# Kernel optimization log

Hardware: AMD Instinct MI355X
Metric: run time of the kernel (lower is better)

Reference implementation:

```python
import jax, jax.numpy as jnp
import numpy as np

EMBED = 256
HEADS = 8
SR = 2
RED = 2


def setup_inputs() -> dict:
    key = jax.random.key(0)
    ks = jax.random.split(key, 12)
    N, B, C = 1024, 64, EMBED
    inp = {
        "query": jax.random.normal(ks[0], (N, B, C), jnp.float32),
        "H": 32,
        "W": 32,
        "key": jax.random.normal(ks[1], (N, B, C), jnp.float32),
        "value": jax.random.normal(ks[2], (N, B, C), jnp.float32),
        # parameters
        "in_proj_weight": jax.random.normal(ks[3], (3 * C, C), jnp.float32) * (1.0 / np.sqrt(C)),
        "in_proj_bias": jnp.zeros((3 * C,), jnp.float32),
        "sr_w": jax.random.normal(ks[4], (C, C, SR, SR), jnp.float32) * np.sqrt(2.0 / (SR * SR * C)),
        "sr_b": jnp.zeros((C,), jnp.float32),
        "norm_g": jnp.ones((C,), jnp.float32),
        "norm_b": jnp.zeros((C,), jnp.float32),
        "out_w": jax.random.normal(ks[5], (C, C), jnp.float32) * (1.0 / np.sqrt(C)),
        "out_b": jnp.zeros((C,), jnp.float32),
        "se_w1": jax.random.normal(ks[6], (C // RED, C), jnp.float32) * 0.02,
        "se_w2": jax.random.normal(ks[7], (C, C // RED), jnp.float32) * 0.02,
    }
    return inp


def _angles(H, W):
    # get_index: a = (pi/2)*(i//W)/H, b = (pi/2)*(i%W)/W for flattened row-major index
    c = np.pi / 2
    idx = jnp.arange(H * W)
    a = c * (idx // W).astype(jnp.float32) / H
    b = c * (idx % W).astype(jnp.float32) / W
    return a, b


def _layernorm(x, g, b, eps=1e-5):
    mu = jnp.mean(x, -1, keepdims=True)
    var = jnp.mean(jnp.square(x - mu), -1, keepdims=True)
    return (x - mu) * jax.lax.rsqrt(var + eps) * g + b


def _abs_clamp(t, lo=1e-4, hi=1e4):
    return jnp.clip(jnp.abs(t), lo, hi) * jnp.sign(t)


def reference(query, H, W, key, value, in_proj_weight, in_proj_bias, sr_w, sr_b,
              norm_g, norm_b, out_w, out_b, se_w1, se_w2):
    N, B, C = query.shape
    h = HEADS
    hd = C // h
    scaling = hd ** (-0.5)

    x = jnp.transpose(query, (1, 0, 2))  # (B, N, C)

    # squeeze-excite gate from query: mean over tokens -> fc1 -> relu -> fc2 -> sigmoid
    se = jnp.mean(x, axis=1)                       # (B, C)
    se = jax.nn.sigmoid(jax.nn.relu(se @ se_w1.T) @ se_w2.T)  # (B, C)

    # spatial reduction conv (kernel=stride=sr_ratio) + layernorm for k/v source
    x_img = jnp.transpose(x, (0, 2, 1)).reshape(B, C, H, W)
    xr = jax.lax.conv_general_dilated(
        x_img, sr_w, window_strides=(SR, SR), padding="VALID",
        dimension_numbers=("NCHW", "OIHW", "NCHW"))
    xr = xr + sr_b[None, :, None, None]
    Hs, Ws = H // SR, W // SR
    Ns = Hs * Ws
    xr = jnp.transpose(xr.reshape(B, C, Ns), (0, 2, 1))  # (B, Ns, C)
    xr = _layernorm(xr, norm_g, norm_b)

    Wq, Wk, Wv = in_proj_weight[:C], in_proj_weight[C:2 * C], in_proj_weight[2 * C:]
    bq, bk, bv = in_proj_bias[:C], in_proj_bias[C:2 * C], in_proj_bias[2 * C:]

    def split_heads(t):  # (B, L, C) -> (B*h, L, hd)
        Bb, L, _ = t.shape
        return jnp.transpose(t.reshape(Bb, L, h, hd), (0, 2, 1, 3)).reshape(Bb * h, L, hd)

    q = split_heads((x @ Wq.T + bq) * scaling)
    k = split_heads(xr @ Wk.T + bk)
    v = split_heads(xr @ Wv.T + bv)

    q = jax.nn.relu(q)
    k = jax.nn.relu(k)

    # cosFormer-2d "sum" reweighting: cos(a_i - a_j) + cos(b_i - b_j)
    a, b = _angles(H, W)       # (N,)
    a2, b2 = _angles(Hs, Ws)   # (Ns,)

    def reweight(t, aa, bb):  # (BH, L, hd), angles (L,) -> (BH, L, 4*hd)
        aa = aa[None, :, None]
        bb = bb[None, :, None]
        return jnp.concatenate(
            [t * jnp.cos(aa), t * jnp.sin(aa), t * jnp.cos(bb), t * jnp.sin(bb)], axis=-1)

    q_ = reweight(q, a, b)     # (BH, N, 4hd)
    k_ = reweight(k, a2, b2)   # (BH, Ns, 4hd)

    # linear attention: never materialize the NxNs matrix
    kv = jnp.einsum("bnd,bnm->bdm", k_, v)             # (BH, 4hd, hd)
    denom = jnp.einsum("bnd,bd->bn", q_, k_.sum(1))    # (BH, N)
    denom = _abs_clamp(denom)
    attn = jnp.einsum("bnd,bdm->bnm", q_, kv) / denom[..., None]  # (BH, N, hd)

    attn = jnp.transpose(attn.reshape(B, h, N, hd), (0, 2, 1, 3)).reshape(B, N, C)
    out = attn @ out_w.T + out_b            # (B, N, C)
    out = out * se[:, None, :]              # SE channel gating
    return jnp.transpose(out, (1, 0, 2))    # (N, B, C)
```

## Files before the change

kernel.cpp:

```cpp
#include <hip/hip_runtime.h>

#define NTOK 1024
#define NB   64
#define CD   256
#define NHEAD 8
#define HDIM 32
#define NS 256
#define NBC 16384

typedef __attribute__((ext_vector_type(8))) short short8v;
typedef __attribute__((ext_vector_type(4))) short short4v;
typedef __attribute__((ext_vector_type(4))) float f32x4;

__device__ __forceinline__ unsigned bfr(float x){
  unsigned u = __float_as_uint(x);
  return (u + 0x7fffu + ((u>>16)&1u)) >> 16;
}
__device__ __forceinline__ void split2(float x, short &h, short &l){
  unsigned hu = bfr(x);
  float hf = __uint_as_float(hu << 16);
  unsigned lu = bfr(x - hf);
  h = (short)hu; l = (short)lu;
}

__global__ __launch_bounds__(256) void k_pre(const float* __restrict__ ipw, const float* __restrict__ ow,
                                             const float* __restrict__ srw,
                                             short* __restrict__ Wih, short* __restrict__ Wil,
                                             short* __restrict__ Woh, short* __restrict__ Wol,
                                             short* __restrict__ Wsh, short* __restrict__ Wsl,
                                             float* __restrict__ t1, float* __restrict__ t2,
                                             const float* __restrict__ query, float* __restrict__ part){
  int bid = blockIdx.x, t = threadIdx.x;
  if (bid < 256){
    int u = bid*256 + t;
    float xs[8];
    short* dh; short* dl; int dof;
    if (u < 24576){
      int n = u >> 5, off = (u & 31)*8;
      const float* s = ipw + n*CD + off;
      #pragma unroll
      for (int i=0;i<8;++i) xs[i] = s[i];
      dh = Wih; dl = Wil; dof = n*CD + off;
    } else if (u < 32768){
      int v = u - 24576;
      int n = v >> 5, off = (v & 31)*8;
      const float* s = ow + n*CD + off;
      #pragma unroll
      for (int i=0;i<8;++i) xs[i] = s[i];
      dh = Woh; dl = Wol; dof = n*CD + off;
    } else {
      int v = u - 32768;
      int n = v >> 7, koff = (v & 127)*8;
      int g = koff >> 8, cin0 = koff & 255;
      #pragma unroll
      for (int i=0;i<8;++i) xs[i] = srw[n*1024 + (cin0+i)*4 + g];
      dh = Wsh; dl = Wsl; dof = n*1024 + koff;
    }
    short8v h, l;
    #pragma unroll
    for (int i=0;i<8;++i){ short a,b; split2(xs[i],a,b); h[i]=a; l[i]=b; }
    *(short8v*)(dh + dof) = h;
    *(short8v*)(dl + dof) = l;
  } else if (bid < 260){
    int n = (bid-256)*256 + t;
    const float c = 1.57079632679489662f;
    float aa = c * (float)(n >> 5) / 32.0f;
    float bb = c * (float)(n & 31) / 32.0f;
    t1[n*4+0]=cosf(aa); t1[n*4+1]=sinf(aa); t1[n*4+2]=cosf(bb); t1[n*4+3]=sinf(bb);
    if (n < 256){
      float a2 = c * (float)(n >> 4) / 16.0f;
      float b2 = c * (float)(n & 15) / 16.0f;
      t2[n*4+0]=cosf(a2); t2[n*4+1]=sinf(a2); t2[n*4+2]=cosf(b2); t2[n*4+3]=sinf(b2);
    }
  } else {
    int vb_ = bid - 260;
    int b = vb_ >> 2, qr = vb_ & 3;
    const float* qp = query + (qr*256)*NBC + b*CD + t;
    float s0=0.f,s1=0.f,s2=0.f,s3=0.f;
    for (int n=0;n<256;n+=4){
      s0 += qp[(n  )*NBC];
      s1 += qp[(n+1)*NBC];
      s2 += qp[(n+2)*NBC];
      s3 += qp[(n+3)*NBC];
    }
    part[vb_*256 + t] = (s0+s1)+(s2+s3);
  }
}

__global__ __launch_bounds__(256) void k_mid(const float* __restrict__ qf,
                                             const short* __restrict__ Wsh, const short* __restrict__ Wsl,
                                             const float* __restrict__ srb, float* __restrict__ xr,
                                             const short* __restrict__ Wih, const short* __restrict__ Wil,
                                             const float* __restrict__ ipb,
                                             short* __restrict__ Qbh, short* __restrict__ Qbl,
                                             const float* __restrict__ part, const float* __restrict__ w1,
                                             const float* __restrict__ w2, float* __restrict__ se){
  __shared__ __align__(16) short smem[16384];
  int bid = blockIdx.x, t = threadIdx.x;
  if (bid < 512){
    short* Ah = smem;
    short* Al = smem + 2048;
    short* Bh = smem + 4096;
    short* Bl = smem + 8192;
    int mblk = bid >> 1, nblk = bid & 1;
    int m0 = mblk*64, n0 = nblk*128;
    int b = mblk >> 2;
    int pos0 = m0 & 255;
    int wave = t>>6, lane = t&63;
    int wm = wave>>1, wn = wave&1;
    int q = lane>>4, r = lane&15;
    int ra = t>>2, pa = (t&3)*8;
    int posA = pos0 + ra, hs = posA>>4, ws2 = posA&15;
    const f32x4 fz = {0.f,0.f,0.f,0.f};
    f32x4 acc[2][4];
    #pragma unroll
    for (int s=0;s<2;++s)
      #pragma unroll
      for (int tt=0;tt<4;++tt) acc[s][tt] = fz;
    for (int kc=0; kc<32; ++kc){
      int g = kc>>3, cin0 = (kc&7)*32;
      int gh = g>>1, gw = g&1;
      int tok = (2*hs+gh)*32 + 2*ws2 + gw;
      const float* src = qf + (size_t)tok*NBC + b*CD + cin0 + pa;
      float4 fa = *(const float4*)src;
      float4 fb = *(const float4*)(src+4);
      float xs[8] = {fa.x,fa.y,fa.z,fa.w,fb.x,fb.y,fb.z,fb.w};
      short8v hh, ll;
      #pragma unroll
      for (int i=0;i<8;++i){ short a0,b0; split2(xs[i],a0,b0); hh[i]=a0; ll[i]=b0; }
      *(short8v*)(Ah + ra*32 + pa) = hh;
      *(short8v*)(Al + ra*32 + pa) = ll;
      int ko = kc*32;
      #pragma unroll
      for (int rep=0; rep<2; ++rep){
        int rr = ra + rep*64;
        int gb = (n0 + rr)*1024 + ko + pa;
        *(short8v*)(Bh + rr*32 + pa) = *(const short8v*)(Wsh + gb);
        *(short8v*)(Bl + rr*32 + pa) = *(const short8v*)(Wsl + gb);
      }
      __syncthreads();
      short8v ah[2], al[2];
      #pragma unroll
      for (int s=0;s<2;++s){
        int row = wm*32 + s*16 + r;
        ah[s] = *(const short8v*)(Ah + row*32 + q*8);
        al[s] = *(const short8v*)(Al + row*32 + q*8);
      }
      #pragma unroll
      for (int tt=0;tt<4;++tt){
        int brow = wn*64 + tt*16 + r;
        short8v bh = *(const short8v*)(Bh + brow*32 + q*8);
        short8v bl = *(const short8v*)(Bl + brow*32 + q*8);
        #pragma unroll
        for (int s=0;s<2;++s){
          acc[s][tt] = __builtin_amdgcn_mfma_f32_16x16x32_bf16(ah[s], bh, acc[s][tt], 0,0,0);
          acc[s][tt] = __builtin_amdgcn_mfma_f32_16x16x32_bf16(ah[s], bl, acc[s][tt], 0,0,0);
          acc[s][tt] = __builtin_amdgcn_mfma_f32_16x16x32_bf16(al[s], bh, acc[s][tt], 0,0,0);
        }
      }
      __syncthreads();
    }
    #pragma unroll
    for (int s=0;s<2;++s){
      #pragma unroll
      for (int tt=0;tt<4;++tt){
        int c = n0 + wn*64 + tt*16 + r;
        float bias = srb[c];
        #pragma unroll
        for (int i=0;i<4;++i){
          int m = m0 + wm*32 + s*16 + q*4 + i;
          xr[m*CD + c] = acc[s][tt][i] + bias;
        }
      }
    }
  } else if (bid < 1536){
    short* Ah = smem;
    short* Al = smem + 4096;
    short* Bh = smem + 8192;
    short* Bl = smem + 12288;
    int qb_ = bid - 512;
    int mblk = qb_ >> 1, nblk = qb_ & 1;
    int m0 = mblk*128, n0 = nblk*128;
    int wave = t>>6, lane = t&63;
    int wm = wave>>1, wn = wave&1;
    int q = lane>>4, r = lane&15;
    int cr = t>>2, cp = (t&3)*8;
    int cpS = (((t&3) ^ ((cr>>1)&3)))*8;
    int sw8 = ((r>>1)&3)*8;
    const f32x4 fz = {0.f,0.f,0.f,0.f};
    f32x4 acc[4][4];
    #pragma unroll
    for (int s=0;s<4;++s)
      #pragma unroll
      for (int tt=0;tt<4;++tt) acc[s][tt] = fz;
    for (int kc=0; kc<8; ++kc){
      int ko = kc*32;
      #pragma unroll
      for (int rep=0; rep<2; ++rep){
        int rr = cr + rep*64;
        int m = m0 + rr;
        const float* src = qf + (size_t)(m & 1023)*NBC + (m >> 10)*CD + ko + cp;
        float4 fa = *(const float4*)src;
        float4 fb = *(const float4*)(src+4);
        float xs[8] = {fa.x,fa.y,fa.z,fa.w,fb.x,fb.y,fb.z,fb.w};
        short8v hh, ll;
        #pragma unroll
        for (int i=0;i<8;++i){ short a0,b0; split2(xs[i],a0,b0); hh[i]=a0; ll[i]=b0; }
        *(short8v*)(Ah + rr*32 + cpS) = hh;
        *(short8v*)(Al + rr*32 + cpS) = ll;
        int gb = (n0 + rr)*CD + ko + cp;
        *(short8v*)(Bh + rr*32 + cpS) = *(const short8v*)(Wih + gb);
        *(short8v*)(Bl + rr*32 + cpS) = *(const short8v*)(Wil + gb);
      }
      __syncthreads();
      short8v ah[4], al[4];
      #pragma unroll
      for (int s=0;s<4;++s){
        int row = wm*64 + s*16 + r;
        ah[s] = *(const short8v*)(Ah + row*32 + ((q*8)^sw8));
        al[s] = *(const short8v*)(Al + row*32 + ((q*8)^sw8));
      }
      #pragma unroll
      for (int tt=0;tt<4;++tt){
        int brow = wn*64 + tt*16 + r;
        short8v bh = *(const short8v*)(Bh + brow*32 + ((q*8)^sw8));
        short8v bl = *(const short8v*)(Bl + brow*32 + ((q*8)^sw8));
        #pragma unroll
        for (int s=0;s<4;++s){
          acc[s][tt] = __builtin_amdgcn_mfma_f32_16x16x32_bf16(ah[s], bh, acc[s][tt], 0,0,0);
          acc[s][tt] = __builtin_amdgcn_mfma_f32_16x16x32_bf16(ah[s], bl, acc[s][tt], 0,0,0);
          acc[s][tt] = __builtin_amdgcn_mfma_f32_16x16x32_bf16(al[s], bh, acc[s][tt], 0,0,0);
        }
      }
      __syncthreads();
    }
    const float sc = 0.17677669529663687f;
    short* T = smem;
    #pragma unroll
    for (int s=0;s<4;++s){
      #pragma unroll
      for (int tt=0;tt<4;++tt){
        int c_loc = wn*64 + tt*16 + r;
        int chunk = c_loc >> 3, cb = c_loc & 7;
        float bias = ipb[n0 + c_loc];
        #pragma unroll
        for (int i=0;i<4;++i){
          int m_loc = wm*64 + s*16 + q*4 + i;
          float val = fmaxf(acc[s][tt][i] + bias, 0.f)*sc;
          unsigned hu = bfr(val);
          T[m_loc*128 + ((chunk ^ (m_loc&7))<<3) + cb] = (short)hu;
          acc[s][tt][i] = val - __uint_as_float(hu<<16);
        }
      }
    }
    __syncthreads();
    {
      int mrl = (lane>>2);
      int ccl = lane&3;
      #pragma unroll
      for (int e=0;e<8;++e){
        int hl = e&3, mg = e>>2;
        int m_loc = wave*32 + mg*16 + mrl;
        int cc16 = hl*4 + ccl;
        short8v v = *(const short8v*)(T + m_loc*128 + ((cc16 ^ (m_loc&7))<<3));
        *(short8v*)(Qbh + ((size_t)((n0>>5)+hl))*2097152 + (size_t)(m0+m_loc)*32 + ccl*8) = v;
      }
    }
    __syncthreads();
    #pragma unroll
    for (int s=0;s<4;++s){
      #pragma unroll
      for (int tt=0;tt<4;++tt){
        int c_loc = wn*64 + tt*16 + r;
        int chunk = c_loc >> 3, cb = c_loc & 7;
        #pragma unroll
        for (int i=0;i<4;++i){
          int m_loc = wm*64 + s*16 + q*4 + i;
          T[m_loc*128 + ((chunk ^ (m_loc&7))<<3) + cb] = (short)bfr(acc[s][tt][i]);
        }
      }
    }
    __syncthreads();
    {
      int mrl = (lane>>2);
      int ccl = lane&3;
      #pragma unroll
      for (int e=0;e<8;++e){
        int hl = e&3, mg = e>>2;
        int m_loc = wave*32 + mg*16 + mrl;
        int cc16 = hl*4 + ccl;
        short8v v = *(const short8v*)(T + m_loc*128 + ((cc16 ^ (m_loc&7))<<3));
        *(short8v*)(Qbl + ((size_t)((n0>>5)+hl))*2097152 + (size_t)(m0+m_loc)*32 + ccl*8) = v;
      }
    }
  } else {
    float* sm = (float*)smem;
    float* s1s = sm + 256;
    int b = bid - 1536;
    float s = (part[(b*4+0)*256+t]+part[(b*4+1)*256+t])+(part[(b*4+2)*256+t]+part[(b*4+3)*256+t]);
    sm[t] = s*(1.0f/1024.0f);
    __syncthreads();
    if (t < 128){
      float a = 0.f;
      const float* wr = w1 + t*256;
      for (int c=0;c<256;c+=4){
        float4 wf = *(const float4*)(wr+c);
        a += sm[c]*wf.x + sm[c+1]*wf.y + sm[c+2]*wf.z + sm[c+3]*wf.w;
      }
      s1s[t] = fmaxf(a, 0.f);
    }
    __syncthreads();
    float a = 0.f;
    const float* wr2 = w2 + t*128;
    for (int c=0;c<128;c+=4){
      float4 wf = *(const float4*)(wr2+c);
      a += s1s[c]*wf.x + s1s[c+1]*wf.y + s1s[c+2]*wf.z + s1s[c+3]*wf.w;
    }
    se[b*256+t] = 1.0f/(1.0f+expf(-a));
  }
}

__global__ __launch_bounds__(256) void k_ln(const float* __restrict__ xr, const float* __restrict__ g,
                                            const float* __restrict__ bta, short* __restrict__ Xh,
                                            short* __restrict__ Xl){
  int wv = threadIdx.x >> 6, lane = threadIdx.x & 63;
  int row = blockIdx.x*4 + wv;
  float4 v = ((const float4*)(xr + row*CD))[lane];
  float s = (v.x+v.y)+(v.z+v.w);
  #pragma unroll
  for (int off=1; off<64; off<<=1) s += __shfl_xor(s, off, 64);
  float mu = s * (1.0f/256.0f);
  float dx=v.x-mu, dy=v.y-mu, dz=v.z-mu, dw=v.w-mu;
  float s2 = (dx*dx+dy*dy)+(dz*dz+dw*dw);
  #pragma unroll
  for (int off=1; off<64; off<<=1) s2 += __shfl_xor(s2, off, 64);
  float inv = 1.0f / sqrtf(s2*(1.0f/256.0f) + 1e-5f);
  float4 gr = ((const float4*)g)[lane];
  float4 br = ((const float4*)bta)[lane];
  float o0 = dx*inv*gr.x + br.x;
  float o1 = dy*inv*gr.y + br.y;
  float o2 = dz*inv*gr.z + br.z;
  float o3 = dw*inv*gr.w + br.w;
  short4v h, l; short a0,b0;
  split2(o0,a0,b0); h[0]=a0; l[0]=b0;
  split2(o1,a0,b0); h[1]=a0; l[1]=b0;
  split2(o2,a0,b0); h[2]=a0; l[2]=b0;
  split2(o3,a0,b0); h[3]=a0; l[3]=b0;
  *(short4v*)(Xh + row*CD + lane*4) = h;
  *(short4v*)(Xl + row*CD + lane*4) = l;
}

__global__ __launch_bounds__(256) void k_kvproj(const short* __restrict__ Xh, const short* __restrict__ Xl,
                                                const short* __restrict__ Wkh, const short* __restrict__ Wkl,
                                                const float* __restrict__ ipb, float* __restrict__ kb,
                                                float* __restrict__ vb){
  __shared__ __align__(16) short Ah[128*32];
  __shared__ __align__(16) short Al[128*32];
  __shared__ __align__(16) short Bh[128*32];
  __shared__ __align__(16) short Bl[128*32];
  int mblk = blockIdx.x >> 2, nblk = blockIdx.x & 3;
  int m0 = mblk*128, n0 = nblk*128;
  int t = threadIdx.x, wave = t>>6, lane = t&63;
  int wm = wave>>1, wn = wave&1;
  int q = lane>>4, r = lane&15;
  int cr = t>>2, cp = (t&3)*8;
  const f32x4 fz = {0.f,0.f,0.f,0.f};
  f32x4 acc[4][4];
  #pragma unroll
  for (int s=0;s<4;++s)
    #pragma unroll
    for (int tt=0;tt<4;++tt) acc[s][tt] = fz;
  for (int kc=0; kc<8; ++kc){
    int ko = kc*32;
    #pragma unroll
    for (int rep=0; rep<2; ++rep){
      int rr = cr + rep*64;
      int ga = (m0 + rr)*CD + ko + cp;
      *(short8v*)(Ah + rr*32 + cp) = *(const short8v*)(Xh + ga);
      *(short8v*)(Al + rr*32 + cp) = *(const short8v*)(Xl + ga);
      int gb = (n0 + rr)*CD + ko + cp;
      *(short8v*)(Bh + rr*32 + cp) = *(const short8v*)(Wkh + gb);
      *(short8v*)(Bl + rr*32 + cp) = *(const short8v*)(Wkl + gb);
    }
    __syncthreads();
    short8v ah[4], al[4];
    #pragma unroll
    for (int s=0;s<4;++s){
      int row = wm*64 + s*16 + r;
      ah[s] = *(const short8v*)(Ah + row*32 + q*8);
      al[s] = *(const short8v*)(Al + row*32 + q*8);
    }
    #pragma unroll
    for (int tt=0;tt<4;++tt){
      int brow = wn*64 + tt*16 + r;
      short8v bh = *(const short8v*)(Bh + brow*32 + q*8);
      short8v bl = *(const short8v*)(Bl + brow*32 + q*8);
      #pragma unroll
      for (int s=0;s<4;++s){
        acc[s][tt] = __builtin_amdgcn_mfma_f32_16x16x32_bf16(ah[s], bh, acc[s][tt], 0,0,0);
        acc[s][tt] = __builtin_amdgcn_mfma_f32_16x16x32_bf16(ah[s], bl, acc[s][tt], 0,0,0);
        acc[s][tt] = __builtin_amdgcn_mfma_f32_16x16x32_bf16(al[s], bh, acc[s][tt], 0,0,0);
      }
    }
    __syncthreads();
  }
  #pragma unroll
  for (int s=0;s<4;++s){
    #pragma unroll
    for (int tt=0;tt<4;++tt){
      int c = n0 + wn*64 + tt*16 + r;
      float bias = ipb[256 + c];
      #pragma unroll
      for (int i=0;i<4;++i){
        int m = m0 + wm*64 + s*16 + q*4 + i;
        float v = acc[s][tt][i] + bias;
        if (c < 256) kb[m*CD + c] = fmaxf(v, 0.f);
        else         vb[m*CD + (c-256)] = v;
      }
    }
  }
}

__global__ __launch_bounds__(256) void k_kvattn(const float* __restrict__ kb, const float* __restrict__ vbuf,
                                                const float* __restrict__ t2,
                                                const short* __restrict__ Qbh, const short* __restrict__ Qbl,
                                                const float* __restrict__ t1,
                                                short* __restrict__ Ath, short* __restrict__ Atl){
  __shared__ __align__(16) short Bh[144*32];
  __shared__ __align__(16) short Bl[144*32];
  __shared__ __align__(16) short Ah[256*32];
  __shared__ __align__(16) short Al[256*32];
  int bh = blockIdx.x, b = bh>>3, h = bh&7;
  int t = threadIdx.x, lane = t&63, wave = t>>6;
  int q = lane>>4, r = lane&15;
  {
    int jq = t >> 5, m = t & 31;
    float acc[4][4];
    #pragma unroll
    for (int p=0;p<4;++p){ acc[p][0]=0.f; acc[p][1]=0.f; acc[p][2]=0.f; acc[p][3]=0.f; }
    const float* kbase = kb + h*HDIM + jq*4;
    const float* vbase = vbuf + h*HDIM + m;
    for (int n=0;n<256;++n){
      int ro = (b*NS + n)*CD;
      float4 k4 = *(const float4*)(kbase + ro);
      float vv = vbase[ro];
      float4 tt = *(const float4*)(t2 + n*4);
      float tv[4] = {tt.x, tt.y, tt.z, tt.w};
      float kk[4] = {k4.x, k4.y, k4.z, k4.w};
      #pragma unroll
      for (int p=0;p<4;++p){
        float tp = tv[p]*vv;
        #pragma unroll
        for (int jj=0;jj<4;++jj) acc[p][jj] += tp*kk[jj];
      }
    }
    #pragma unroll
    for (int p=0;p<4;++p){
      short4v h4, l4;
      #pragma unroll
      for (int jj=0;jj<4;++jj){ short a,bq; split2(acc[p][jj],a,bq); h4[jj]=a; l4[jj]=bq; }
      *(short4v*)(Bh + (p*32+m)*32 + jq*4) = h4;
      *(short4v*)(Bl + (p*32+m)*32 + jq*4) = l4;
    }
    if (t < 128){
      int p = t >> 5, j = t & 31;
      float s=0.f;
      const float* kp = kb + h*HDIM + j;
      for (int n=0;n<256;++n) s += t2[n*4+p]*kp[(b*NS+n)*CD];
      short a,bq; split2(s,a,bq);
      Bh[(128+p)*32 + j] = a;
      Bl[(128+p)*32 + j] = bq;
    } else {
      int idx = t - 128;
      #pragma unroll
      for (int ii=0;ii<3;++ii){
        Bh[4224 + idx*3 + ii] = 0;
        Bl[4224 + idx*3 + ii] = 0;
      }
    }
  }
  __syncthreads();
  short8v bf_h[9], bf_l[9];
  #pragma unroll
  for (int nt=0; nt<9; ++nt){
    int row = nt*16 + r;
    bf_h[nt] = *(const short8v*)(Bh + row*32 + q*8);
    bf_l[nt] = *(const short8v*)(Bl + row*32 + q*8);
  }
  const short* qh_base = Qbh + ((size_t)h*65536 + (size_t)b*1024)*32;
  const short* ql_base = Qbl + ((size_t)h*65536 + (size_t)b*1024)*32;
  const f32x4 fz = {0.f,0.f,0.f,0.f};
  for (int u=0; u<4; ++u){
    __syncthreads();
    {
      const short8v* sh = (const short8v*)(qh_base + (u*256 + t)*32);
      const short8v* sl = (const short8v*)(ql_base + (u*256 + t)*32);
      short8v* dh = (short8v*)(Ah + t*32);
      short8v* dl = (short8v*)(Al + t*32);
      #pragma unroll
      for (int i=0;i<4;++i){ dh[i]=sh[i]; dl[i]=sl[i]; }
    }
    __syncthreads();
    #pragma unroll
    for (int mi=0; mi<4; ++mi){
      int mt = wave*4 + mi;
      short8v ah = *(const short8v*)(Ah + (mt*16 + r)*32 + q*8);
      short8v al = *(const short8v*)(Al + (mt*16 + r)*32 + q*8);
      f32x4 acc[9];
      #pragma unroll
      for (int nt=0;nt<9;++nt) acc[nt]=fz;
      #pragma unroll
      for (int nt=0;nt<9;++nt){
        acc[nt] = __builtin_amdgcn_mfma_f32_16x16x32_bf16(ah, bf_h[nt], acc[nt],0,0,0);
        acc[nt] = __builtin_amdgcn_mfma_f32_16x16x32_bf16(ah, bf_l[nt], acc[nt],0,0,0);
        acc[nt] = __builtin_amdgcn_mfma_f32_16x16x32_bf16(al, bf_h[nt], acc[nt],0,0,0);
      }
      int nbase = u*256 + mt*16 + q*4;
      int src = lane & 48;
      #pragma unroll
      for (int i=0;i<4;++i){
        int n = nbase + i;
        float4 tv = *(const float4*)(t1 + n*4);
        float dp0 = __shfl(acc[8][i], src+0, 64);
        float dp1 = __shfl(acc[8][i], src+1, 64);
        float dp2 = __shfl(acc[8][i], src+2, 64);
        float dp3 = __shfl(acc[8][i], src+3, 64);
        float den = tv.x*dp0 + tv.y*dp1 + tv.z*dp2 + tv.w*dp3;
        float a0 = tv.x*acc[0][i] + tv.y*acc[2][i] + tv.z*acc[4][i] + tv.w*acc[6][i];
        float a1 = tv.x*acc[1][i] + tv.y*acc[3][i] + tv.z*acc[5][i] + tv.w*acc[7][i];
        float sgn = (den>0.f) ? 1.f : ((den<0.f)? -1.f : 0.f);
        float ad = fminf(fmaxf(fabsf(den), 1e-4f), 1e4f);
        float inv = (den != 0.f) ? 1.0f/(ad*sgn) : 0.f;
        float o0 = a0*inv, o1 = a1*inv;
        int mrow = b*NTOK + n;
        short h0,l0,h1,l1;
        split2(o0,h0,l0); split2(o1,h1,l1);
        Ath[mrow*CD + h*HDIM + r]      = h0;
        Atl[mrow*CD + h*HDIM + r]      = l0;
        Ath[mrow*CD + h*HDIM + 16 + r] = h1;
        Atl[mrow*CD + h*HDIM + 16 + r] = l1;
      }
    }
  }
}

__global__ __launch_bounds__(256) void k_outproj(const short* __restrict__ Ath, const short* __restrict__ Atl,
                                                 const short* __restrict__ Woh, const short* __restrict__ Wol,
                                                 const float* __restrict__ obv, const float* __restrict__ se,
                                                 float* __restrict__ dout){
  __shared__ __align__(16) short Ah[128*32];
  __shared__ __align__(16) short Al[128*32];
  __shared__ __align__(16) short Bh[128*32];
  __shared__ __align__(16) short Bl[128*32];
  int mblk = blockIdx.x >> 1, nblk = blockIdx.x & 1;
  int m0 = mblk*128, n0 = nblk*128;
  int t = threadIdx.x, wave = t>>6, lane = t&63;
  int wm = wave>>1, wn = wave&1;
  int q = lane>>4, r = lane&15;
  int cr = t>>2, cp = (t&3)*8;
  const f32x4 fz = {0.f,0.f,0.f,0.f};
  f32x4 acc[4][4];
  #pragma unroll
  for (int s=0;s<4;++s)
    #pragma unroll
    for (int tt=0;tt<4;++tt) acc[s][tt] = fz;
  for (int kc=0; kc<8; ++kc){
    int ko = kc*32;
    #pragma unroll
    for (int rep=0; rep<2; ++rep){
      int rr = cr + rep*64;
      int ga = (m0 + rr)*CD + ko + cp;
      *(short8v*)(Ah + rr*32 + cp) = *(const short8v*)(Ath + ga);
      *(short8v*)(Al + rr*32 + cp) = *(const short8v*)(Atl + ga);
      int gb = (n0 + rr)*CD + ko + cp;
      *(short8v*)(Bh + rr*32 + cp) = *(const short8v*)(Woh + gb);
      *(short8v*)(Bl + rr*32 + cp) = *(const short8v*)(Wol + gb);
    }
    __syncthreads();
    short8v ah[4], al[4];
    #pragma unroll
    for (int s=0;s<4;++s){
      int row = wm*64 + s*16 + r;
      ah[s] = *(const short8v*)(Ah + row*32 + q*8);
      al[s] = *(const short8v*)(Al + row*32 + q*8);
    }
    #pragma unroll
    for (int tt=0;tt<4;++tt){
      int brow = wn*64 + tt*16 + r;
      short8v bh = *(const short8v*)(Bh + brow*32 + q*8);
      short8v bl = *(const short8v*)(Bl + brow*32 + q*8);
      #pragma unroll
      for (int s=0;s<4;++s){
        acc[s][tt] = __builtin_amdgcn_mfma_f32_16x16x32_bf16(ah[s], bh, acc[s][tt], 0,0,0);
        acc[s][tt] = __builtin_amdgcn_mfma_f32_16x16x32_bf16(ah[s], bl, acc[s][tt], 0,0,0);
        acc[s][tt] = __builtin_amdgcn_mfma_f32_16x16x32_bf16(al[s], bh, acc[s][tt], 0,0,0);
      }
    }
    __syncthreads();
  }
  #pragma unroll
  for (int s=0;s<4;++s){
    #pragma unroll
    for (int tt=0;tt<4;++tt){
      int c = n0 + wn*64 + tt*16 + r;
      float bias = obv[c];
      #pragma unroll
      for (int i=0;i<4;++i){
        int m = m0 + wm*64 + s*16 + q*4 + i;
        int bb = m >> 10, ntok = m & 1023;
        float sev = se[bb*CD + c];
        dout[(ntok*NB + bb)*CD + c] = (acc[s][tt][i] + bias)*sev;
      }
    }
  }
}

extern "C" void kernel_launch(void* const* d_in, const int* in_sizes, int n_in,
                              void* d_out, int out_size, void* d_ws, size_t ws_size,
                              hipStream_t stream) {
  const float* query = (const float*)d_in[0];
  const float* ipw = (const float*)d_in[5];
  const float* ipb = (const float*)d_in[6];
  const float* srw = (const float*)d_in[7];
  const float* srb = (const float*)d_in[8];
  const float* ng  = (const float*)d_in[9];
  const float* nbb = (const float*)d_in[10];
  const float* ow  = (const float*)d_in[11];
  const float* obv = (const float*)d_in[12];
  const float* sw1 = (const float*)d_in[13];
  const float* sw2 = (const float*)d_in[14];
  float* dout = (float*)d_out;
  float* ws = (float*)d_ws;

  short* Qbh  = (short*)ws;
  short* Qbl  = (short*)(ws + 8388608);
  float* R1   = ws + 16777216;
  float* kb   = R1;
  float* vb   = R1 + 4194304;
  short* Ath  = (short*)(R1 + 8388608);
  short* Atl  = (short*)(ws + 33554432);
  float* xr   = ws + 33554432;
  short* Xh   = (short*)(ws + 37748736);
  short* Xl   = (short*)(ws + 39845888);
  float* part = ws + 44302336;
  float* se   = ws + 44367872;
  float* t1   = ws + 44384256;
  float* t2   = ws + 44388352;
  short* Wih  = (short*)(ws + 44389376);
  short* Wil  = (short*)(ws + 44487680);
  short* Woh  = (short*)(ws + 44585984);
  short* Wol  = (short*)(ws + 44618752);
  short* Wsh  = (short*)(ws + 44651520);
  short* Wsl  = (short*)(ws + 44782592);

  k_pre   <<<516,  256,0,stream>>>(ipw, ow, srw, Wih, Wil, Woh, Wol, Wsh, Wsl, t1, t2, query, part);
  k_mid   <<<1600, 256,0,stream>>>(query, Wsh, Wsl, srb, xr, Wih, Wil, ipb, Qbh, Qbl, part, sw1, sw2, se);
  k_ln    <<<4096, 256,0,stream>>>(xr, ng, nbb, Xh, Xl);
  k_kvproj<<<512,  256,0,stream>>>(Xh, Xl, Wih + 256*CD, Wil + 256*CD, ipb, kb, vb);
  k_kvattn<<<512,  256,0,stream>>>(kb, vb, t2, Qbh, Qbl, t1, Ath, Atl);
  k_outproj<<<1024,256,0,stream>>>(Ath, Atl, Woh, Wol, obv, se, dout);
}
```

Baseline: 430.0 us.

## Fuse weight prep, layernorm, and SE into neighboring kernels to cut launches

Removes the separate weight-conversion prologue by having the SR-conv and Q-projection GEMMs split fp32 weights on the fly, and moves the remaining K/V/out weight conversion, angle tables and query partial sums into extra blocks of k_mid. LayerNorm is folded into k_kvproj, which computes per-row statistics and normalizes while staging A tiles, so the Xh/Xl intermediate is gone. The SE MLP moves into extra blocks of k_kvattn. This cuts the launch count from six to four and drops intermediate traffic, at the cost of redundant weight splitting per tile and strided srw loads.

```diff
diff --git a/kernel.cpp b/kernel.cpp
--- a/kernel.cpp
+++ b/kernel.cpp
@@ -23,78 +23,16 @@
   h = (short)hu; l = (short)lu;
 }
 
-__global__ __launch_bounds__(256) void k_pre(const float* __restrict__ ipw, const float* __restrict__ ow,
+__global__ __launch_bounds__(256) void k_mid(const float* __restrict__ qf,
                                              const float* __restrict__ srw,
+                                             const float* __restrict__ srb, float* __restrict__ xr,
+                                             const float* __restrict__ ipw, const float* __restrict__ ipb,
+                                             short* __restrict__ Qbh, short* __restrict__ Qbl,
+                                             const float* __restrict__ ow,
                                              short* __restrict__ Wih, short* __restrict__ Wil,
                                              short* __restrict__ Woh, short* __restrict__ Wol,
-                                             short* __restrict__ Wsh, short* __restrict__ Wsl,
                                              float* __restrict__ t1, float* __restrict__ t2,
-                                             const float* __restrict__ query, float* __restrict__ part){
-  int bid = blockIdx.x, t = threadIdx.x;
-  if (bid < 256){
-    int u = bid*256 + t;
-    float xs[8];
-    short* dh; short* dl; int dof;
-    if (u < 24576){
-      int n = u >> 5, off = (u & 31)*8;
-      const float* s = ipw + n*CD + off;
-      #pragma unroll
-      for (int i=0;i<8;++i) xs[i] = s[i];
-      dh = Wih; dl = Wil; dof = n*CD + off;
-    } else if (u < 32768){
-      int v = u - 24576;
-      int n = v >> 5, off = (v & 31)*8;
-      const float* s = ow + n*CD + off;
-      #pragma unroll
-      for (int i=0;i<8;++i) xs[i] = s[i];
-      dh = Woh; dl = Wol; dof = n*CD + off;
-    } else {
-      int v = u - 32768;
-      int n = v >> 7, koff = (v & 127)*8;
-      int g = koff >> 8, cin0 = koff & 255;
-      #pragma unroll
-      for (int i=0;i<8;++i) xs[i] = srw[n*1024 + (cin0+i)*4 + g];
-      dh = Wsh; dl = Wsl; dof = n*1024 + koff;
-    }
-    short8v h, l;
-    #pragma unroll
-    for (int i=0;i<8;++i){ short a,b; split2(xs[i],a,b); h[i]=a; l[i]=b; }
-    *(short8v*)(dh + dof) = h;
-    *(short8v*)(dl + dof) = l;
-  } else if (bid < 260){
-    int n = (bid-256)*256 + t;
-    const float c = 1.57079632679489662f;
-    float aa = c * (float)(n >> 5) / 32.0f;
-    float bb = c * (float)(n & 31) / 32.0f;
-    t1[n*4+0]=cosf(aa); t1[n*4+1]=sinf(aa); t1[n*4+2]=cosf(bb); t1[n*4+3]=sinf(bb);
-    if (n < 256){
-      float a2 = c * (float)(n >> 4) / 16.0f;
-      float b2 = c * (float)(n & 15) / 16.0f;
-      t2[n*4+0]=cosf(a2); t2[n*4+1]=sinf(a2); t2[n*4+2]=cosf(b2); t2[n*4+3]=sinf(b2);
-    }
-  } else {
-    int vb_ = bid - 260;
-    int b = vb_ >> 2, qr = vb_ & 3;
-    const float* qp = query + (qr*256)*NBC + b*CD + t;
-    float s0=0.f,s1=0.f,s2=0.f,s3=0.f;
-    for (int n=0;n<256;n+=4){
-      s0 += qp[(n  )*NBC];
-      s1 += qp[(n+1)*NBC];
-      s2 += qp[(n+2)*NBC];
-      s3 += qp[(n+3)*NBC];
-    }
-    part[vb_*256 + t] = (s0+s1)+(s2+s3);
-  }
-}
-
-__global__ __launch_bounds__(256) void k_mid(const float* __restrict__ qf,
-                                             const short* __restrict__ Wsh, const short* __restrict__ Wsl,
-                                             const float* __restrict__ srb, float* __restrict__ xr,
-                                             const short* __restrict__ Wih, const short* __restrict__ Wil,
-                                             const float* __restrict__ ipb,
-                                             short* __restrict__ Qbh, short* __restrict__ Qbl,
-                                             const float* __restrict__ part, const float* __restrict__ w1,
-                                             const float* __restrict__ w2, float* __restrict__ se){
+                                             float* __restrict__ part){
   __shared__ __align__(16) short smem[16384];
   int bid = blockIdx.x, t = threadIdx.x;
   if (bid < 512){
@@ -130,13 +68,15 @@
       for (int i=0;i<8;++i){ short a0,b0; split2(xs[i],a0,b0); hh[i]=a0; ll[i]=b0; }
       *(short8v*)(Ah + ra*32 + pa) = hh;
       *(short8v*)(Al + ra*32 + pa) = ll;
-      int ko = kc*32;
       #pragma unroll
       for (int rep=0; rep<2; ++rep){
         int rr = ra + rep*64;
-        int gb = (n0 + rr)*1024 + ko + pa;
-        *(short8v*)(Bh + rr*32 + pa) = *(const short8v*)(Wsh + gb);
-        *(short8v*)(Bl + rr*32 + pa) = *(const short8v*)(Wsl + gb);
+        const float* wsrc = srw + (size_t)(n0+rr)*1024 + (size_t)(cin0+pa)*4 + g;
+        short8v wh8, wl8;
+        #pragma unroll
+        for (int i=0;i<8;++i){ short a0,b0; split2(wsrc[i*4],a0,b0); wh8[i]=a0; wl8[i]=b0; }
+        *(short8v*)(Bh + rr*32 + pa) = wh8;
+        *(short8v*)(Bl + rr*32 + pa) = wl8;
       }
       __syncthreads();
       short8v ah[2], al[2];
@@ -208,9 +148,15 @@
         for (int i=0;i<8;++i){ short a0,b0; split2(xs[i],a0,b0); hh[i]=a0; ll[i]=b0; }
         *(short8v*)(Ah + rr*32 + cpS) = hh;
         *(short8v*)(Al + rr*32 + cpS) = ll;
-        int gb = (n0 + rr)*CD + ko + cp;
-        *(short8v*)(Bh + rr*32 + cpS) = *(const short8v*)(Wih + gb);
-        *(short8v*)(Bl + rr*32 + cpS) = *(const short8v*)(Wil + gb);
+        const float* wsrc = ipw + (size_t)(n0+rr)*CD + ko + cp;
+        float4 wa = *(const float4*)wsrc;
+        float4 wb = *(const float4*)(wsrc+4);
+        float wsv[8] = {wa.x,wa.y,wa.z,wa.w,wb.x,wb.y,wb.z,wb.w};
+        short8v wh8, wl8;
+        #pragma unroll
+        for (int i=0;i<8;++i){ short a0,b0; split2(wsv[i],a0,b0); wh8[i]=a0; wl8[i]=b0; }
+        *(short8v*)(Bh + rr*32 + cpS) = wh8;
+        *(short8v*)(Bl + rr*32 + cpS) = wl8;
       }
       __syncthreads();
       short8v ah[4], al[4];
@@ -293,64 +239,52 @@
         *(short8v*)(Qbl + ((size_t)((n0>>5)+hl))*2097152 + (size_t)(m0+m_loc)*32 + ccl*8) = v;
       }
     }
+  } else if (bid < 1632){
+    int u = (bid-1536)*256 + t;
+    const float* s; short* dh; short* dl; int dof;
+    if (u < 16384){
+      int n = 256 + (u >> 5), off = (u & 31)*8;
+      s = ipw + n*CD + off;
+      dh = Wih; dl = Wil; dof = n*CD + off;
+    } else {
+      int v = u - 16384;
+      int n = v >> 5, off = (v & 31)*8;
+      s = ow + n*CD + off;
+      dh = Woh; dl = Wol; dof = n*CD + off;
+    }
+    short8v h, l;
+    #pragma unroll
+    for (int i=0;i<8;++i){ short a,b; split2(s[i],a,b); h[i]=a; l[i]=b; }
+    *(short8v*)(dh + dof) = h;
+    *(short8v*)(dl + dof) = l;
+  } else if (bid < 1636){
+    int n = (bid-1632)*256 + t;
+    const float c = 1.57079632679489662f;
+    float aa = c * (float)(n >> 5) / 32.0f;
+    float bb = c * (float)(n & 31) / 32.0f;
+    t1[n*4+0]=cosf(aa); t1[n*4+1]=sinf(aa); t1[n*4+2]=cosf(bb); t1[n*4+3]=sinf(bb);
+    if (n < 256){
+      float a2 = c * (float)(n >> 4) / 16.0f;
+      float b2 = c * (float)(n & 15) / 16.0f;
+      t2[n*4+0]=cosf(a2); t2[n*4+1]=sinf(a2); t2[n*4+2]=cosf(b2); t2[n*4+3]=sinf(b2);
+    }
   } else {
-    float* sm = (float*)smem;
-    float* s1s = sm + 256;
-    int b = bid - 1536;
-    float s = (part[(b*4+0)*256+t]+part[(b*4+1)*256+t])+(part[(b*4+2)*256+t]+part[(b*4+3)*256+t]);
-    sm[t] = s*(1.0f/1024.0f);
-    __syncthreads();
-    if (t < 128){
-      float a = 0.f;
-      const float* wr = w1 + t*256;
-      for (int c=0;c<256;c+=4){
-        float4 wf = *(const float4*)(wr+c);
-        a += sm[c]*wf.x + sm[c+1]*wf.y + sm[c+2]*wf.z + sm[c+3]*wf.w;
-      }
-      s1s[t] = fmaxf(a, 0.f);
-    }
-    __syncthreads();
-    float a = 0.f;
-    const float* wr2 = w2 + t*128;
-    for (int c=0;c<128;c+=4){
-      float4 wf = *(const float4*)(wr2+c);
-      a += s1s[c]*wf.x + s1s[c+1]*wf.y + s1s[c+2]*wf.z + s1s[c+3]*wf.w;
-    }
-    se[b*256+t] = 1.0f/(1.0f+expf(-a));
+    int vb_ = bid - 1636;
+    int b = vb_ >> 2, qr = vb_ & 3;
+    const float* qp = qf + (qr*256)*NBC + b*CD + t;
+    float s0=0.f,s1=0.f,s2=0.f,s3=0.f;
+    for (int n=0;n<256;n+=4){
+      s0 += qp[(n  )*NBC];
+      s1 += qp[(n+1)*NBC];
+      s2 += qp[(n+2)*NBC];
+      s3 += qp[(n+3)*NBC];
+    }
+    part[vb_*256 + t] = (s0+s1)+(s2+s3);
   }
 }
 
-__global__ __launch_bounds__(256) void k_ln(const float* __restrict__ xr, const float* __restrict__ g,
-                                            const float* __restrict__ bta, short* __restrict__ Xh,
-                                            short* __restrict__ Xl){
-  int wv = threadIdx.x >> 6, lane = threadIdx.x & 63;
-  int row = blockIdx.x*4 + wv;
-  float4 v = ((const float4*)(xr + row*CD))[lane];
-  float s = (v.x+v.y)+(v.z+v.w);
-  #pragma unroll
-  for (int off=1; off<64; off<<=1) s += __shfl_xor(s, off, 64);
-  float mu = s * (1.0f/256.0f);
-  float dx=v.x-mu, dy=v.y-mu, dz=v.z-mu, dw=v.w-mu;
-  float s2 = (dx*dx+dy*dy)+(dz*dz+dw*dw);
-  #pragma unroll
-  for (int off=1; off<64; off<<=1) s2 += __shfl_xor(s2, off, 64);
-  float inv = 1.0f / sqrtf(s2*(1.0f/256.0f) + 1e-5f);
-  float4 gr = ((const float4*)g)[lane];
-  float4 br = ((const float4*)bta)[lane];
-  float o0 = dx*inv*gr.x + br.x;
-  float o1 = dy*inv*gr.y + br.y;
-  float o2 = dz*inv*gr.z + br.z;
-  float o3 = dw*inv*gr.w + br.w;
-  short4v h, l; short a0,b0;
-  split2(o0,a0,b0); h[0]=a0; l[0]=b0;
-  split2(o1,a0,b0); h[1]=a0; l[1]=b0;
-  split2(o2,a0,b0); h[2]=a0; l[2]=b0;
-  split2(o3,a0,b0); h[3]=a0; l[3]=b0;
-  *(short4v*)(Xh + row*CD + lane*4) = h;
-  *(short4v*)(Xl + row*CD + lane*4) = l;
-}
-
-__global__ __launch_bounds__(256) void k_kvproj(const short* __restrict__ Xh, const short* __restrict__ Xl,
+__global__ __launch_bounds__(256) void k_kvproj(const float* __restrict__ xr, const float* __restrict__ lng,
+                                                const float* __restrict__ lnb,
                                                 const short* __restrict__ Wkh, const short* __restrict__ Wkl,
                                                 const float* __restrict__ ipb, float* __restrict__ kb,
                                                 float* __restrict__ vb){
@@ -358,12 +292,29 @@
   __shared__ __align__(16) short Al[128*32];
   __shared__ __align__(16) short Bh[128*32];
   __shared__ __align__(16) short Bl[128*32];
+  __shared__ float mu_s[128];
+  __shared__ float inv_s[128];
   int mblk = blockIdx.x >> 2, nblk = blockIdx.x & 3;
   int m0 = mblk*128, n0 = nblk*128;
   int t = threadIdx.x, wave = t>>6, lane = t&63;
   int wm = wave>>1, wn = wave&1;
   int q = lane>>4, r = lane&15;
   int cr = t>>2, cp = (t&3)*8;
+  for (int rr8=0; rr8<32; ++rr8){
+    int rr = rr8*4 + wave;
+    float4 v = ((const float4*)(xr + (size_t)(m0+rr)*CD))[lane];
+    float s = (v.x+v.y)+(v.z+v.w);
+    #pragma unroll
+    for (int off=1; off<64; off<<=1) s += __shfl_xor(s, off, 64);
+    float mu = s * (1.0f/256.0f);
+    float dx=v.x-mu, dy=v.y-mu, dz=v.z-mu, dw=v.w-mu;
+    float s2 = (dx*dx+dy*dy)+(dz*dz+dw*dw);
+    #pragma unroll
+    for (int off=1; off<64; off<<=1) s2 += __shfl_xor(s2, off, 64);
+    float inv = 1.0f / sqrtf(s2*(1.0f/256.0f) + 1e-5f);
+    if (lane==0){ mu_s[rr]=mu; inv_s[rr]=inv; }
+  }
+  __syncthreads();
   const f32x4 fz = {0.f,0.f,0.f,0.f};
   f32x4 acc[4][4];
   #pragma unroll
@@ -375,9 +326,25 @@
     #pragma unroll
     for (int rep=0; rep<2; ++rep){
       int rr = cr + rep*64;
-      int ga = (m0 + rr)*CD + ko + cp;
-      *(short8v*)(Ah + rr*32 + cp) = *(const short8v*)(Xh + ga);
-      *(short8v*)(Al + rr*32 + cp) = *(const short8v*)(Xl + ga);
+      const float* src = xr + (size_t)(m0+rr)*CD + ko + cp;
+      float4 fa = *(const float4*)src;
+      float4 fb = *(const float4*)(src+4);
+      float xs[8] = {fa.x,fa.y,fa.z,fa.w,fb.x,fb.y,fb.z,fb.w};
+      float4 g0 = *(const float4*)(lng + ko + cp);
+      float4 g1 = *(const float4*)(lng + ko + cp + 4);
+      float4 b0 = *(const float4*)(lnb + ko + cp);
+      float4 b1 = *(const float4*)(lnb + ko + cp + 4);
+      float gv[8] = {g0.x,g0.y,g0.z,g0.w,g1.x,g1.y,g1.z,g1.w};
+      float bv[8] = {b0.x,b0.y,b0.z,b0.w,b1.x,b1.y,b1.z,b1.w};
+      float mu = mu_s[rr], inv = inv_s[rr];
+      short8v hh, ll;
+      #pragma unroll
+      for (int i=0;i<8;++i){
+        short a0,bq; split2(((xs[i]-mu)*inv)*gv[i] + bv[i], a0,bq);
+        hh[i]=a0; ll[i]=bq;
+      }
+      *(short8v*)(Ah + rr*32 + cp) = hh;
+      *(short8v*)(Al + rr*32 + cp) = ll;
       int gb = (n0 + rr)*CD + ko + cp;
       *(short8v*)(Bh + rr*32 + cp) = *(const short8v*)(Wkh + gb);
       *(short8v*)(Bl + rr*32 + cp) = *(const short8v*)(Wkl + gb);
@@ -425,13 +392,43 @@
                                                 const float* __restrict__ t2,
                                                 const short* __restrict__ Qbh, const short* __restrict__ Qbl,
                                                 const float* __restrict__ t1,
-                                                short* __restrict__ Ath, short* __restrict__ Atl){
-  __shared__ __align__(16) short Bh[144*32];
-  __shared__ __align__(16) short Bl[144*32];
-  __shared__ __align__(16) short Ah[256*32];
-  __shared__ __align__(16) short Al[256*32];
+                                                short* __restrict__ Ath, short* __restrict__ Atl,
+                                                const float* __restrict__ part, const float* __restrict__ w1,
+                                                const float* __restrict__ w2, float* __restrict__ se){
+  __shared__ __align__(16) char arena[51200];
+  int t = threadIdx.x;
+  if (blockIdx.x >= 512){
+    float* sm = (float*)arena;
+    float* s1s = sm + 256;
+    int b = blockIdx.x - 512;
+    float s = (part[(b*4+0)*256+t]+part[(b*4+1)*256+t])+(part[(b*4+2)*256+t]+part[(b*4+3)*256+t]);
+    sm[t] = s*(1.0f/1024.0f);
+    __syncthreads();
+    if (t < 128){
+      float a = 0.f;
+      const float* wr = w1 + t*256;
+      for (int c=0;c<256;c+=4){
+        float4 wf = *(const float4*)(wr+c);
+        a += sm[c]*wf.x + sm[c+1]*wf.y + sm[c+2]*wf.z + sm[c+3]*wf.w;
+      }
+      s1s[t] = fmaxf(a, 0.f);
+    }
+    __syncthreads();
+    float a = 0.f;
+    const float* wr2 = w2 + t*128;
+    for (int c=0;c<128;c+=4){
+      float4 wf = *(const float4*)(wr2+c);
+      a += s1s[c]*wf.x + s1s[c+1]*wf.y + s1s[c+2]*wf.z + s1s[c+3]*wf.w;
+    }
+    se[b*256+t] = 1.0f/(1.0f+expf(-a));
+    return;
+  }
+  short* Bh = (short*)arena;
+  short* Bl = (short*)(arena + 9216);
+  short* Ah = (short*)(arena + 18432);
+  short* Al = (short*)(arena + 34816);
   int bh = blockIdx.x, b = bh>>3, h = bh&7;
-  int t = threadIdx.x, lane = t&63, wave = t>>6;
+  int lane = t&63, wave = t>>6;
   int q = lane>>4, r = lane&15;
   {
     int jq = t >> 5, m = t & 31;
@@ -640,8 +637,6 @@
   short* Ath  = (short*)(R1 + 8388608);
   short* Atl  = (short*)(ws + 33554432);
   float* xr   = ws + 33554432;
-  short* Xh   = (short*)(ws + 37748736);
-  short* Xl   = (short*)(ws + 39845888);
   float* part = ws + 44302336;
   float* se   = ws + 44367872;
   float* t1   = ws + 44384256;
@@ -650,13 +645,10 @@
   short* Wil  = (short*)(ws + 44487680);
   short* Woh  = (short*)(ws + 44585984);
   short* Wol  = (short*)(ws + 44618752);
-  short* Wsh  = (short*)(ws + 44651520);
-  short* Wsl  = (short*)(ws + 44782592);
-
-  k_pre   <<<516,  256,0,stream>>>(ipw, ow, srw, Wih, Wil, Woh, Wol, Wsh, Wsl, t1, t2, query, part);
-  k_mid   <<<1600, 256,0,stream>>>(query, Wsh, Wsl, srb, xr, Wih, Wil, ipb, Qbh, Qbl, part, sw1, sw2, se);
-  k_ln    <<<4096, 256,0,stream>>>(xr, ng, nbb, Xh, Xl);
-  k_kvproj<<<512,  256,0,stream>>>(Xh, Xl, Wih + 256*CD, Wil + 256*CD, ipb, kb, vb);
-  k_kvattn<<<512,  256,0,stream>>>(kb, vb, t2, Qbh, Qbl, t1, Ath, Atl);
+
+  k_mid   <<<1892, 256,0,stream>>>(query, srw, srb, xr, ipw, ipb, Qbh, Qbl, ow,
+                                   Wih, Wil, Woh, Wol, t1, t2, part);
+  k_kvproj<<<512,  256,0,stream>>>(xr, ng, nbb, Wih + 256*CD, Wil + 256*CD, ipb, kb, vb);
+  k_kvattn<<<576,  256,0,stream>>>(kb, vb, t2, Qbh, Qbl, t1, Ath, Atl, part, sw1, sw2, se);
   k_outproj<<<1024,256,0,stream>>>(Ath, Atl, Woh, Wol, obv, se, dout);
 }
```

Result: slower. 549.3 us (+27.7%).
